# Kernel tuning notes

Hardware: AMD Instinct MI355X
Metric: run time of the kernel (lower is better)

Reference implementation:

```python
import jax, jax.numpy as jnp
import numpy as np

D_MODEL = 1024
NUM_HEADS = 16
D_HEAD = D_MODEL // NUM_HEADS
BATCH = 2
SEQ = 2048


def setup_inputs() -> dict:
    key = jax.random.key(0)
    ks = jax.random.split(key, 5)
    std = 0.02
    return {
        "x": jax.random.normal(ks[0], (BATCH, SEQ, D_MODEL), dtype=jnp.float32),
        "Wq": jax.random.normal(ks[1], (D_MODEL, D_MODEL), dtype=jnp.float32) * std,
        "Wk": jax.random.normal(ks[2], (D_MODEL, D_MODEL), dtype=jnp.float32) * std,
        "Wv": jax.random.normal(ks[3], (D_MODEL, D_MODEL), dtype=jnp.float32) * std,
        "Wo": jax.random.normal(ks[4], (D_MODEL, D_MODEL), dtype=jnp.float32) * std,
    }


def reference(x, Wq, Wk, Wv, Wo):
    batch, seq_len, d_model = x.shape
    h, dh = NUM_HEADS, D_HEAD

    def split_heads(W):
        # x @ W.T -> (b, s, d) -> (b, h, s, dh)
        p = jnp.einsum('bsd,ed->bse', x, W)
        return p.reshape(batch, seq_len, h, dh).transpose(0, 2, 1, 3)

    Q = split_heads(Wq)
    K = split_heads(Wk)
    V = split_heads(Wv)

    scale = 1.0 / jnp.sqrt(jnp.asarray(dh, dtype=x.dtype))
    scores = jnp.einsum('bhqd,bhkd->bhqk', Q, K) * scale
    causal = jnp.tril(jnp.ones((seq_len, seq_len), dtype=bool))
    scores = jnp.where(causal, scores, -jnp.inf)
    attn = jax.nn.softmax(scores, axis=-1)
    out = jnp.einsum('bhqk,bhkd->bhqd', attn, V)  # (b, h, s, dh)
    out = out.transpose(0, 2, 1, 3).reshape(batch, seq_len, d_model)
    return jnp.einsum('bsd,ed->bse', out, Wo)
```

## Files before the change

kernel.cpp:

```cpp
#include <hip/hip_runtime.h>

#define D_MODEL 1024
#define NUM_HEADS 16
#define D_HEAD 64
#define BATCH 2
#define SEQ 2048
#define MTOT (BATCH * SEQ)
#define PLANE ((size_t)MTOT * D_MODEL)
#define QSCALE 0.1803368801f

typedef unsigned short us;
typedef __bf16 bf16x8 __attribute__((ext_vector_type(8)));
typedef float floatx4 __attribute__((ext_vector_type(4)));

__device__ __forceinline__ unsigned int f2bf(float f) {
  union { float f; unsigned int i; } v; v.f = f;
  unsigned int r = v.i + 0x7FFFu + ((v.i >> 16) & 1u);
  return r >> 16;
}
__device__ __forceinline__ unsigned int f2bf_tr(float f) {
  union { float f; unsigned int i; } v; v.f = f;
  return v.i >> 16;
}

__global__ __launch_bounds__(256) void convert_all(const float* __restrict__ x,
                                                   const float* __restrict__ Wq,
                                                   const float* __restrict__ Wk,
                                                   const float* __restrict__ Wv,
                                                   us* __restrict__ xbf,
                                                   us* __restrict__ Wqkv) {
  const int i = blockIdx.x * 256 + threadIdx.x;
  const float* src;
  us* dst;
  if (i < (1 << 20)) {
    src = x + (size_t)i * 4;
    dst = xbf + (size_t)i * 4;
  } else {
    const int j = i - (1 << 20);
    const int w = j >> 18;
    const int o = j & ((1 << 18) - 1);
    const float* ws = (w == 0) ? Wq : (w == 1) ? Wk : Wv;
    src = ws + (size_t)o * 4;
    dst = Wqkv + (size_t)w * (D_MODEL * D_MODEL) + (size_t)o * 4;
  }
  float4 v = *(const float4*)src;
  uint2 pk;
  pk.x = f2bf(v.x) | (f2bf(v.y) << 16);
  pk.y = f2bf(v.z) | (f2bf(v.w) << 16);
  *(uint2*)dst = pk;
}

__global__ __launch_bounds__(256) void convert_bf16(const float* __restrict__ src,
                                                    us* __restrict__ dst, int n4) {
  int i = blockIdx.x * 256 + threadIdx.x;
  if (i >= n4) return;
  float4 v = *(const float4*)(src + (size_t)i * 4);
  uint2 pk;
  pk.x = f2bf(v.x) | (f2bf(v.y) << 16);
  pk.y = f2bf(v.z) | (f2bf(v.w) << 16);
  *(uint2*)(dst + (size_t)i * 4) = pk;
}

template <int CMODE>
__global__ __launch_bounds__(256) void gemm_mfma(const us* __restrict__ A,
                                                 const us* __restrict__ B,
                                                 void* __restrict__ Cv,
                                                 int M, int N, int K) {
  __shared__ __bf16 As[128 * 32];
  __shared__ __bf16 Bs[128 * 32];
  const int tid = threadIdx.x;
  const int wid = tid >> 6;
  const int lane = tid & 63;
  const int bm = blockIdx.y * 128;
  const int bn = blockIdx.x * 128;
  const int wm = (wid & 1) * 64;
  const int wn = (wid >> 1) * 64;
  const int lr = lane & 15;
  const int quad = lane >> 4;

  floatx4 acc[4][4] = {};
  const int cb0 = wid * 128;

  for (int k0 = 0; k0 < K; k0 += 32) {
    __syncthreads();
#pragma unroll
    for (int p = 0; p < 2; ++p) {
      const int cb = cb0 + p * 64;
      const int c = cb + lane;
      const us* ga = A + (size_t)(bm + (c >> 2)) * K + (k0 + (c & 3) * 8);
      const us* gb = B + (size_t)(bn + (c >> 2)) * K + (k0 + (c & 3) * 8);
      __builtin_amdgcn_global_load_lds((const __attribute__((address_space(1))) void*)ga,
                                       (__attribute__((address_space(3))) void*)(&As[cb * 8]),
                                       16, 0, 0);
      __builtin_amdgcn_global_load_lds((const __attribute__((address_space(1))) void*)gb,
                                       (__attribute__((address_space(3))) void*)(&Bs[cb * 8]),
                                       16, 0, 0);
    }
    __syncthreads();

    bf16x8 a[4], b[4];
#pragma unroll
    for (int i = 0; i < 4; ++i)
      a[i] = *(const bf16x8*)&As[(wm + i * 16 + lr) * 32 + quad * 8];
#pragma unroll
    for (int j = 0; j < 4; ++j)
      b[j] = *(const bf16x8*)&Bs[(wn + j * 16 + lr) * 32 + quad * 8];
#pragma unroll
    for (int i = 0; i < 4; ++i)
#pragma unroll
      for (int j = 0; j < 4; ++j)
        acc[i][j] = __builtin_amdgcn_mfma_f32_16x16x32_bf16(a[i], b[j], acc[i][j], 0, 0, 0);
  }

#pragma unroll
  for (int i = 0; i < 4; ++i) {
#pragma unroll
    for (int j = 0; j < 4; ++j) {
      const int col = bn + wn + j * 16 + lr;
      if constexpr (CMODE == 1) {
        us* dst = (us*)Cv;
        const int plane = col >> 10;
        if (plane < 2) {
          const float s = (plane == 0) ? QSCALE : 1.0f;
#pragma unroll
          for (int r = 0; r < 4; ++r) {
            const int row = bm + wm + i * 16 + quad * 4 + r;
            dst[(size_t)plane * PLANE + (size_t)row * 1024 + (col & 1023)] =
                (us)f2bf(acc[i][j][r] * s);
          }
        } else {
          const int d = col & 63;
          const int hh = (col >> 6) & 15;
          const int row0 = bm + wm + i * 16 + quad * 4;
          const int bb = row0 >> 11;
          const int ss = row0 & 2047;
          uint2 pk;
          pk.x = f2bf(acc[i][j][0]) | (f2bf(acc[i][j][1]) << 16);
          pk.y = f2bf(acc[i][j][2]) | (f2bf(acc[i][j][3]) << 16);
          *(uint2*)&dst[2 * PLANE + ((size_t)((bb * 16 + hh) * 64 + d)) * 2048 + ss] = pk;
        }
      } else {
#pragma unroll
        for (int r = 0; r < 4; ++r) {
          const int row = bm + wm + i * 16 + quad * 4 + r;
          ((float*)Cv)[(size_t)row * N + col] = acc[i][j][r];
        }
      }
    }
  }
}

#define ASTR 72

__global__ __launch_bounds__(256, 2) void attn_mfma(const us* __restrict__ Qb,
                                                    const us* __restrict__ Kb,
                                                    const us* __restrict__ Vtg,
                                                    us* __restrict__ Ob) {
  const int bx = blockIdx.x;
  const int b = bx >> 8;
  const int idx = bx & 255;
  const int h = idx >> 4;
  const int s0 = idx & 15;
  const int strip = b ? (15 - s0) : s0;
  const int q0 = strip * 128;
  const int ntiles = 2 * strip + 2;
  const int tid = threadIdx.x;
  const int w = tid >> 6;
  const int lane = tid & 63;
  const int lr = lane & 15;
  const int quad = lane >> 4;

  __shared__ us Ks[2][64 * ASTR];
  __shared__ us Vs[2][64 * ASTR];
  __shared__ us Ps[8 * 16 * ASTR];

  bf16x8 qa[2][2];
#pragma unroll
  for (int g = 0; g < 2; ++g) {
    const us* qp = Qb + (size_t)(b * SEQ + q0 + w * 32 + g * 16 + lr) * D_MODEL + h * D_HEAD;
    qa[g][0] = *(const bf16x8*)(qp + quad * 8);
    qa[g][1] = *(const bf16x8*)(qp + 32 + quad * 8);
  }

  floatx4 oacc[2][4] = {};
  floatx4 lacc[2] = {};
  bf16x8 ones;
#pragma unroll
  for (int i = 0; i < 8; ++i) ones[i] = (__bf16)1.0f;

  const us* kbase = Kb + (size_t)(b * SEQ) * D_MODEL + h * D_HEAD;
  const us* vbase = Vtg + (size_t)((b * 16 + h) * 64) * 2048;
  us* const pg0 = &Ps[(w * 2 + 0) * 16 * ASTR];
  us* const pg1 = &Ps[(w * 2 + 1) * 16 * ASTR];

  uint4 kreg[2], vreg[2];
#pragma unroll
  for (int p = 0; p < 2; ++p) {
    const int c = tid + 256 * p;
    kreg[p] = *(const uint4*)(kbase + (size_t)(c >> 3) * D_MODEL + (c & 7) * 8);
    vreg[p] = *(const uint4*)(vbase + (size_t)(c >> 3) * 2048 + (c & 7) * 8);
  }
#pragma unroll
  for (int p = 0; p < 2; ++p) {
    const int c = tid + 256 * p;
    *(uint4*)&Ks[0][(c >> 3) * ASTR + (c & 7) * 8] = kreg[p];
    *(uint4*)&Vs[0][(c >> 3) * ASTR + (c & 7) * 8] = vreg[p];
  }
  __syncthreads();

  for (int t = 0; t < ntiles; ++t) {
    const int k0 = t * 64;
    const int cur = t & 1;
    const bool more = (t + 1 < ntiles);

    if (more) {
      const int kn = k0 + 64;
#pragma unroll
      for (int p = 0; p < 2; ++p) {
        const int c = tid + 256 * p;
        kreg[p] = *(const uint4*)(kbase + (size_t)(kn + (c >> 3)) * D_MODEL + (c & 7) * 8);
        vreg[p] = *(const uint4*)(vbase + (size_t)(c >> 3) * 2048 + kn + (c & 7) * 8);
      }
    }

#pragma unroll
    for (int jt = 0; jt < 4; ++jt) {
      const bf16x8 kb0 = *(const bf16x8*)&Ks[cur][(jt * 16 + lr) * ASTR + quad * 8];
      const bf16x8 kb1 = *(const bf16x8*)&Ks[cur][(jt * 16 + lr) * ASTR + 32 + quad * 8];
#pragma unroll
      for (int g = 0; g < 2; ++g) {
        floatx4 s = {};
        s = __builtin_amdgcn_mfma_f32_16x16x32_bf16(kb0, qa[g][0], s, 0, 0, 0);
        s = __builtin_amdgcn_mfma_f32_16x16x32_bf16(kb1, qa[g][1], s, 0, 0, 0);
        const int grow = q0 + w * 32 + g * 16;
        const int kb = k0 + jt * 16 + quad * 4;
        const bool needMask = (k0 + jt * 16 + 15 > grow);
        float p[4];
#pragma unroll
        for (int r = 0; r < 4; ++r) {
          float e = __builtin_amdgcn_exp2f(s[r]);
          if (needMask && (kb + r > grow + lr)) e = 0.f;
          p[r] = e;
        }
        uint2 pk;
        pk.x = f2bf_tr(p[0]) | (f2bf_tr(p[1]) << 16);
        pk.y = f2bf_tr(p[2]) | (f2bf_tr(p[3]) << 16);
        us* const pg = g ? pg1 : pg0;
        *(uint2*)&pg[lr * ASTR + jt * 16 + quad * 4] = pk;
      }
    }

    const bf16x8 pa00 = *(const bf16x8*)&pg0[lr * ASTR + quad * 8];
    const bf16x8 pa01 = *(const bf16x8*)&pg0[lr * ASTR + 32 + quad * 8];
    const bf16x8 pa10 = *(const bf16x8*)&pg1[lr * ASTR + quad * 8];
    const bf16x8 pa11 = *(const bf16x8*)&pg1[lr * ASTR + 32 + quad * 8];
    lacc[0] = __builtin_amdgcn_mfma_f32_16x16x32_bf16(ones, pa00, lacc[0], 0, 0, 0);
    lacc[0] = __builtin_amdgcn_mfma_f32_16x16x32_bf16(ones, pa01, lacc[0], 0, 0, 0);
    lacc[1] = __builtin_amdgcn_mfma_f32_16x16x32_bf16(ones, pa10, lacc[1], 0, 0, 0);
    lacc[1] = __builtin_amdgcn_mfma_f32_16x16x32_bf16(ones, pa11, lacc[1], 0, 0, 0);
#pragma unroll
    for (int nt = 0; nt < 4; ++nt) {
      const bf16x8 vb0 = *(const bf16x8*)&Vs[cur][(nt * 16 + lr) * ASTR + quad * 8];
      const bf16x8 vb1 = *(const bf16x8*)&Vs[cur][(nt * 16 + lr) * ASTR + 32 + quad * 8];
      oacc[0][nt] = __builtin_amdgcn_mfma_f32_16x16x32_bf16(vb0, pa00, oacc[0][nt], 0, 0, 0);
      oacc[0][nt] = __builtin_amdgcn_mfma_f32_16x16x32_bf16(vb1, pa01, oacc[0][nt], 0, 0, 0);
      oacc[1][nt] = __builtin_amdgcn_mfma_f32_16x16x32_bf16(vb0, pa10, oacc[1][nt], 0, 0, 0);
      oacc[1][nt] = __builtin_amdgcn_mfma_f32_16x16x32_bf16(vb1, pa11, oacc[1][nt], 0, 0, 0);
    }

    if (more) {
      const int nxt = cur ^ 1;
#pragma unroll
      for (int p = 0; p < 2; ++p) {
        const int c = tid + 256 * p;
        *(uint4*)&Ks[nxt][(c >> 3) * ASTR + (c & 7) * 8] = kreg[p];
        *(uint4*)&Vs[nxt][(c >> 3) * ASTR + (c & 7) * 8] = vreg[p];
      }
    }
    __syncthreads();
  }

#pragma unroll
  for (int g = 0; g < 2; ++g) {
    us* const pg = g ? pg1 : pg0;
    const int grow = q0 + w * 32 + g * 16;
    const float inv = 1.f / lacc[g][0];
#pragma unroll
    for (int nt = 0; nt < 4; ++nt) {
      uint2 pk;
      pk.x = f2bf_tr(oacc[g][nt][0] * inv) | (f2bf_tr(oacc[g][nt][1] * inv) << 16);
      pk.y = f2bf_tr(oacc[g][nt][2] * inv) | (f2bf_tr(oacc[g][nt][3] * inv) << 16);
      *(uint2*)&pg[lr * ASTR + nt * 16 + quad * 4] = pk;
    }
#pragma unroll
    for (int p = 0; p < 2; ++p) {
      const int c = lane + 64 * p;
      *(uint4*)(Ob + (size_t)(b * SEQ + grow + (c >> 3)) * D_MODEL + h * D_HEAD + (c & 7) * 8) =
          *(const uint4*)&pg[(c >> 3) * ASTR + (c & 7) * 8];
    }
  }
}

extern "C" void kernel_launch(void* const* d_in, const int* in_sizes, int n_in,
                              void* d_out, int out_size, void* d_ws, size_t ws_size,
                              hipStream_t stream) {
  const float* x  = (const float*)d_in[0];
  const float* Wq = (const float*)d_in[1];
  const float* Wk = (const float*)d_in[2];
  const float* Wv = (const float*)d_in[3];
  const float* Wo = (const float*)d_in[4];

  us* xbf = (us*)d_ws;
  us* Qb  = xbf + PLANE;
  us* Kb  = xbf + 2 * PLANE;
  us* Vt  = xbf + 3 * PLANE;
  us* Ab  = xbf;
  us* Wqkv = (us*)d_out;
  us* Wobf = Qb;
  float* out = (float*)d_out;

  const int WN = D_MODEL * D_MODEL;

  convert_all<<<7168, 256, 0, stream>>>(x, Wq, Wk, Wv, xbf, Wqkv);

  gemm_mfma<1><<<dim3(3072 / 128, MTOT / 128), 256, 0, stream>>>(xbf, Wqkv, Qb, MTOT, 3072, D_MODEL);

  attn_mfma<<<512, 256, 0, stream>>>(Qb, Kb, Vt, Ab);

  convert_bf16<<<WN / 4 / 256, 256, 0, stream>>>(Wo, Wobf, WN / 4);
  gemm_mfma<2><<<dim3(D_MODEL / 128, MTOT / 128), 256, 0, stream>>>(Ab, Wobf, out, MTOT, D_MODEL, D_MODEL);
}
```

Baseline: 194.9 us.

## Process paired 64-row causal strips per block for balanced attention work

Each attention block used to handle one 128-row query strip, with strip order reversed across batches to spread load. Now each block handles two 64-row strips, s0 and 31-s0, one after the other, so every block does the same total number of KV tiles. Each wave now owns 16 query rows instead of 32, which halves the per-wave accumulators and the P scratch in shared memory. The cost is that each K/V tile loaded into shared memory now serves only 64 query rows instead of 128, so KV traffic per unit of compute roughly doubles.

Result: slower. 226.0 us (+16.0%).

```diff
diff --git a/kernel.cpp b/kernel.cpp
--- a/kernel.cpp
+++ b/kernel.cpp
@@ -157,13 +157,10 @@
                                                     const us* __restrict__ Vtg,
                                                     us* __restrict__ Ob) {
   const int bx = blockIdx.x;
-  const int b = bx >> 8;
-  const int idx = bx & 255;
-  const int h = idx >> 4;
-  const int s0 = idx & 15;
-  const int strip = b ? (15 - s0) : s0;
-  const int q0 = strip * 128;
-  const int ntiles = 2 * strip + 2;
+  const int s0 = bx & 15;
+  const int bh = bx >> 4;
+  const int b = bh >> 4;
+  const int h = bh & 15;
   const int tid = threadIdx.x;
   const int w = tid >> 6;
   const int lane = tid & 63;
@@ -172,67 +169,66 @@
 
   __shared__ us Ks[2][64 * ASTR];
   __shared__ us Vs[2][64 * ASTR];
-  __shared__ us Ps[8 * 16 * ASTR];
-
-  bf16x8 qa[2][2];
-#pragma unroll
-  for (int g = 0; g < 2; ++g) {
-    const us* qp = Qb + (size_t)(b * SEQ + q0 + w * 32 + g * 16 + lr) * D_MODEL + h * D_HEAD;
-    qa[g][0] = *(const bf16x8*)(qp + quad * 8);
-    qa[g][1] = *(const bf16x8*)(qp + 32 + quad * 8);
-  }
-
-  floatx4 oacc[2][4] = {};
-  floatx4 lacc[2] = {};
-  bf16x8 ones;
-#pragma unroll
-  for (int i = 0; i < 8; ++i) ones[i] = (__bf16)1.0f;
+  __shared__ us Ps[4 * 16 * ASTR];
 
   const us* kbase = Kb + (size_t)(b * SEQ) * D_MODEL + h * D_HEAD;
   const us* vbase = Vtg + (size_t)((b * 16 + h) * 64) * 2048;
-  us* const pg0 = &Ps[(w * 2 + 0) * 16 * ASTR];
-  us* const pg1 = &Ps[(w * 2 + 1) * 16 * ASTR];
-
-  uint4 kreg[2], vreg[2];
-#pragma unroll
-  for (int p = 0; p < 2; ++p) {
-    const int c = tid + 256 * p;
-    kreg[p] = *(const uint4*)(kbase + (size_t)(c >> 3) * D_MODEL + (c & 7) * 8);
-    vreg[p] = *(const uint4*)(vbase + (size_t)(c >> 3) * 2048 + (c & 7) * 8);
-  }
-#pragma unroll
-  for (int p = 0; p < 2; ++p) {
-    const int c = tid + 256 * p;
-    *(uint4*)&Ks[0][(c >> 3) * ASTR + (c & 7) * 8] = kreg[p];
-    *(uint4*)&Vs[0][(c >> 3) * ASTR + (c & 7) * 8] = vreg[p];
-  }
-  __syncthreads();
-
-  for (int t = 0; t < ntiles; ++t) {
-    const int k0 = t * 64;
-    const int cur = t & 1;
-    const bool more = (t + 1 < ntiles);
-
-    if (more) {
-      const int kn = k0 + 64;
-#pragma unroll
-      for (int p = 0; p < 2; ++p) {
-        const int c = tid + 256 * p;
-        kreg[p] = *(const uint4*)(kbase + (size_t)(kn + (c >> 3)) * D_MODEL + (c & 7) * 8);
-        vreg[p] = *(const uint4*)(vbase + (size_t)(c >> 3) * 2048 + kn + (c & 7) * 8);
-      }
-    }
-
-#pragma unroll
-    for (int jt = 0; jt < 4; ++jt) {
-      const bf16x8 kb0 = *(const bf16x8*)&Ks[cur][(jt * 16 + lr) * ASTR + quad * 8];
-      const bf16x8 kb1 = *(const bf16x8*)&Ks[cur][(jt * 16 + lr) * ASTR + 32 + quad * 8];
-#pragma unroll
-      for (int g = 0; g < 2; ++g) {
+  us* const pg = &Ps[w * 16 * ASTR];
+
+  bf16x8 ones;
+#pragma unroll
+  for (int i = 0; i < 8; ++i) ones[i] = (__bf16)1.0f;
+
+  for (int sp = 0; sp < 2; ++sp) {
+    const int strip = sp ? (31 - s0) : s0;
+    const int q0 = strip * 64;
+    const int ntiles = strip + 1;
+    const int grow = q0 + w * 16;
+
+    const us* qp = Qb + (size_t)(b * SEQ + grow + lr) * D_MODEL + h * D_HEAD;
+    const bf16x8 qa0 = *(const bf16x8*)(qp + quad * 8);
+    const bf16x8 qa1 = *(const bf16x8*)(qp + 32 + quad * 8);
+
+    floatx4 oacc[4] = {};
+    floatx4 lacc = {};
+
+    uint4 kreg[2], vreg[2];
+#pragma unroll
+    for (int p = 0; p < 2; ++p) {
+      const int c = tid + 256 * p;
+      kreg[p] = *(const uint4*)(kbase + (size_t)(c >> 3) * D_MODEL + (c & 7) * 8);
+      vreg[p] = *(const uint4*)(vbase + (size_t)(c >> 3) * 2048 + (c & 7) * 8);
+    }
+#pragma unroll
+    for (int p = 0; p < 2; ++p) {
+      const int c = tid + 256 * p;
+      *(uint4*)&Ks[0][(c >> 3) * ASTR + (c & 7) * 8] = kreg[p];
+      *(uint4*)&Vs[0][(c >> 3) * ASTR + (c & 7) * 8] = vreg[p];
+    }
+    __syncthreads();
+
+    for (int t = 0; t < ntiles; ++t) {
+      const int k0 = t * 64;
+      const int cur = t & 1;
+      const bool more = (t + 1 < ntiles);
+
+      if (more) {
+        const int kn = k0 + 64;
+#pragma unroll
+        for (int p = 0; p < 2; ++p) {
+          const int c = tid + 256 * p;
+          kreg[p] = *(const uint4*)(kbase + (size_t)(kn + (c >> 3)) * D_MODEL + (c & 7) * 8);
+          vreg[p] = *(const uint4*)(vbase + (size_t)(c >> 3) * 2048 + kn + (c & 7) * 8);
+        }
+      }
+
+#pragma unroll
+      for (int jt = 0; jt < 4; ++jt) {
+        const bf16x8 kb0 = *(const bf16x8*)&Ks[cur][(jt * 16 + lr) * ASTR + quad * 8];
+        const bf16x8 kb1 = *(const bf16x8*)&Ks[cur][(jt * 16 + lr) * ASTR + 32 + quad * 8];
         floatx4 s = {};
-        s = __builtin_amdgcn_mfma_f32_16x16x32_bf16(kb0, qa[g][0], s, 0, 0, 0);
-        s = __builtin_amdgcn_mfma_f32_16x16x32_bf16(kb1, qa[g][1], s, 0, 0, 0);
-        const int grow = q0 + w * 32 + g * 16;
+        s = __builtin_amdgcn_mfma_f32_16x16x32_bf16(kb0, qa0, s, 0, 0, 0);
+        s = __builtin_amdgcn_mfma_f32_16x16x32_bf16(kb1, qa1, s, 0, 0, 0);
         const int kb = k0 + jt * 16 + quad * 4;
         const bool needMask = (k0 + jt * 16 + 15 > grow);
         float p[4];
@@ -245,51 +241,39 @@
         uint2 pk;
         pk.x = f2bf_tr(p[0]) | (f2bf_tr(p[1]) << 16);
         pk.y = f2bf_tr(p[2]) | (f2bf_tr(p[3]) << 16);
-        us* const pg = g ? pg1 : pg0;
         *(uint2*)&pg[lr * ASTR + jt * 16 + quad * 4] = pk;
       }
-    }
-
-    const bf16x8 pa00 = *(const bf16x8*)&pg0[lr * ASTR + quad * 8];
-    const bf16x8 pa01 = *(const bf16x8*)&pg0[lr * ASTR + 32 + quad * 8];
-    const bf16x8 pa10 = *(const bf16x8*)&pg1[lr * ASTR + quad * 8];
-    const bf16x8 pa11 = *(const bf16x8*)&pg1[lr * ASTR + 32 + quad * 8];
-    lacc[0] = __builtin_amdgcn_mfma_f32_16x16x32_bf16(ones, pa00, lacc[0], 0, 0, 0);
-    lacc[0] = __builtin_amdgcn_mfma_f32_16x16x32_bf16(ones, pa01, lacc[0], 0, 0, 0);
-    lacc[1] = __builtin_amdgcn_mfma_f32_16x16x32_bf16(ones, pa10, lacc[1], 0, 0, 0);
-    lacc[1] = __builtin_amdgcn_mfma_f32_16x16x32_bf16(ones, pa11, lacc[1], 0, 0, 0);
-#pragma unroll
-    for (int nt = 0; nt < 4; ++nt) {
-      const bf16x8 vb0 = *(const bf16x8*)&Vs[cur][(nt * 16 + lr) * ASTR + quad * 8];
-      const bf16x8 vb1 = *(const bf16x8*)&Vs[cur][(nt * 16 + lr) * ASTR + 32 + quad * 8];
-      oacc[0][nt] = __builtin_amdgcn_mfma_f32_16x16x32_bf16(vb0, pa00, oacc[0][nt], 0, 0, 0);
-      oacc[0][nt] = __builtin_amdgcn_mfma_f32_16x16x32_bf16(vb1, pa01, oacc[0][nt], 0, 0, 0);
-      oacc[1][nt] = __builtin_amdgcn_mfma_f32_16x16x32_bf16(vb0, pa10, oacc[1][nt], 0, 0, 0);
-      oacc[1][nt] = __builtin_amdgcn_mfma_f32_16x16x32_bf16(vb1, pa11, oacc[1][nt], 0, 0, 0);
-    }
-
-    if (more) {
-      const int nxt = cur ^ 1;
-#pragma unroll
-      for (int p = 0; p < 2; ++p) {
-        const int c = tid + 256 * p;
-        *(uint4*)&Ks[nxt][(c >> 3) * ASTR + (c & 7) * 8] = kreg[p];
-        *(uint4*)&Vs[nxt][(c >> 3) * ASTR + (c & 7) * 8] = vreg[p];
-      }
-    }
-    __syncthreads();
-  }
-
-#pragma unroll
-  for (int g = 0; g < 2; ++g) {
-    us* const pg = g ? pg1 : pg0;
-    const int grow = q0 + w * 32 + g * 16;
-    const float inv = 1.f / lacc[g][0];
+
+      const bf16x8 pa0 = *(const bf16x8*)&pg[lr * ASTR + quad * 8];
+      const bf16x8 pa1 = *(const bf16x8*)&pg[lr * ASTR + 32 + quad * 8];
+      lacc = __builtin_amdgcn_mfma_f32_16x16x32_bf16(ones, pa0, lacc, 0, 0, 0);
+      lacc = __builtin_amdgcn_mfma_f32_16x16x32_bf16(ones, pa1, lacc, 0, 0, 0);
+#pragma unroll
+      for (int nt = 0; nt < 4; ++nt) {
+        const bf16x8 vb0 = *(const bf16x8*)&Vs[cur][(nt * 16 + lr) * ASTR + quad * 8];
+        const bf16x8 vb1 = *(const bf16x8*)&Vs[cur][(nt * 16 + lr) * ASTR + 32 + quad * 8];
+        oacc[nt] = __builtin_amdgcn_mfma_f32_16x16x32_bf16(vb0, pa0, oacc[nt], 0, 0, 0);
+        oacc[nt] = __builtin_amdgcn_mfma_f32_16x16x32_bf16(vb1, pa1, oacc[nt], 0, 0, 0);
+      }
+
+      if (more) {
+        const int nxt = cur ^ 1;
+#pragma unroll
+        for (int p = 0; p < 2; ++p) {
+          const int c = tid + 256 * p;
+          *(uint4*)&Ks[nxt][(c >> 3) * ASTR + (c & 7) * 8] = kreg[p];
+          *(uint4*)&Vs[nxt][(c >> 3) * ASTR + (c & 7) * 8] = vreg[p];
+        }
+      }
+      __syncthreads();
+    }
+
+    const float inv = 1.f / lacc[0];
 #pragma unroll
     for (int nt = 0; nt < 4; ++nt) {
       uint2 pk;
-      pk.x = f2bf_tr(oacc[g][nt][0] * inv) | (f2bf_tr(oacc[g][nt][1] * inv) << 16);
-      pk.y = f2bf_tr(oacc[g][nt][2] * inv) | (f2bf_tr(oacc[g][nt][3] * inv) << 16);
+      pk.x = f2bf_tr(oacc[nt][0] * inv) | (f2bf_tr(oacc[nt][1] * inv) << 16);
+      pk.y = f2bf_tr(oacc[nt][2] * inv) | (f2bf_tr(oacc[nt][3] * inv) << 16);
       *(uint2*)&pg[lr * ASTR + nt * 16 + quad * 4] = pk;
     }
 #pragma unroll
```

## Make attention kernel persistent with atomic longest-first job queue

Applied to the files above, without the earlier changes.

The attention kernel becomes persistent. 256 blocks each pull (strip, batch, head) jobs from a global atomic counter, ordered so the longest causal strips go first, and the counter is reset inside the conversion kernel. The aim is to balance uneven causal workloads across CUs and remove tail imbalance from static block scheduling. In exchange, the grid is halved, which may cut resident waves per CU and latency hiding. It also adds an atomic plus a barrier per job, and keeps the counter in scratch space inside the output buffer.

New measurement: 226.4 us. 1.16x slower.

```diff
diff --git a/kernel.cpp b/kernel.cpp
--- a/kernel.cpp
+++ b/kernel.cpp
@@ -28,8 +28,10 @@
                                                    const float* __restrict__ Wk,
                                                    const float* __restrict__ Wv,
                                                    us* __restrict__ xbf,
-                                                   us* __restrict__ Wqkv) {
+                                                   us* __restrict__ Wqkv,
+                                                   int* __restrict__ ctr) {
   const int i = blockIdx.x * 256 + threadIdx.x;
+  if (i == 0) *ctr = 0;
   const float* src;
   us* dst;
   if (i < (1 << 20)) {
@@ -151,19 +153,13 @@
 }
 
 #define ASTR 72
+#define NJOBS 512
 
 __global__ __launch_bounds__(256, 2) void attn_mfma(const us* __restrict__ Qb,
                                                     const us* __restrict__ Kb,
                                                     const us* __restrict__ Vtg,
-                                                    us* __restrict__ Ob) {
-  const int bx = blockIdx.x;
-  const int b = bx >> 8;
-  const int idx = bx & 255;
-  const int h = idx >> 4;
-  const int s0 = idx & 15;
-  const int strip = b ? (15 - s0) : s0;
-  const int q0 = strip * 128;
-  const int ntiles = 2 * strip + 2;
+                                                    us* __restrict__ Ob,
+                                                    int* __restrict__ ctr) {
   const int tid = threadIdx.x;
   const int w = tid >> 6;
   const int lane = tid & 63;
@@ -173,130 +169,146 @@
   __shared__ us Ks[2][64 * ASTR];
   __shared__ us Vs[2][64 * ASTR];
   __shared__ us Ps[8 * 16 * ASTR];
-
-  bf16x8 qa[2][2];
-#pragma unroll
-  for (int g = 0; g < 2; ++g) {
-    const us* qp = Qb + (size_t)(b * SEQ + q0 + w * 32 + g * 16 + lr) * D_MODEL + h * D_HEAD;
-    qa[g][0] = *(const bf16x8*)(qp + quad * 8);
-    qa[g][1] = *(const bf16x8*)(qp + 32 + quad * 8);
-  }
-
-  floatx4 oacc[2][4] = {};
-  floatx4 lacc[2] = {};
-  bf16x8 ones;
-#pragma unroll
-  for (int i = 0; i < 8; ++i) ones[i] = (__bf16)1.0f;
-
-  const us* kbase = Kb + (size_t)(b * SEQ) * D_MODEL + h * D_HEAD;
-  const us* vbase = Vtg + (size_t)((b * 16 + h) * 64) * 2048;
+  __shared__ int jslot;
+
   us* const pg0 = &Ps[(w * 2 + 0) * 16 * ASTR];
   us* const pg1 = &Ps[(w * 2 + 1) * 16 * ASTR];
 
-  uint4 kreg[2], vreg[2];
-#pragma unroll
-  for (int p = 0; p < 2; ++p) {
-    const int c = tid + 256 * p;
-    kreg[p] = *(const uint4*)(kbase + (size_t)(c >> 3) * D_MODEL + (c & 7) * 8);
-    vreg[p] = *(const uint4*)(vbase + (size_t)(c >> 3) * 2048 + (c & 7) * 8);
-  }
-#pragma unroll
-  for (int p = 0; p < 2; ++p) {
-    const int c = tid + 256 * p;
-    *(uint4*)&Ks[0][(c >> 3) * ASTR + (c & 7) * 8] = kreg[p];
-    *(uint4*)&Vs[0][(c >> 3) * ASTR + (c & 7) * 8] = vreg[p];
-  }
-  __syncthreads();
-
-  for (int t = 0; t < ntiles; ++t) {
-    const int k0 = t * 64;
-    const int cur = t & 1;
-    const bool more = (t + 1 < ntiles);
-
-    if (more) {
-      const int kn = k0 + 64;
+  bf16x8 ones;
+#pragma unroll
+  for (int i = 0; i < 8; ++i) ones[i] = (__bf16)1.0f;
+
+  for (;;) {
+    if (tid == 0) jslot = atomicAdd(ctr, 1);
+    __syncthreads();
+    const int job = jslot;
+    if (job >= NJOBS) break;
+    const int strip = 15 - (job >> 5);
+    const int slot = job & 31;
+    const int b = slot >> 4;
+    const int h = slot & 15;
+    const int q0 = strip * 128;
+    const int ntiles = 2 * strip + 2;
+
+    const us* kbase = Kb + (size_t)(b * SEQ) * D_MODEL + h * D_HEAD;
+    const us* vbase = Vtg + (size_t)((b * 16 + h) * 64) * 2048;
+
+    bf16x8 qa[2][2];
+#pragma unroll
+    for (int g = 0; g < 2; ++g) {
+      const us* qp = Qb + (size_t)(b * SEQ + q0 + w * 32 + g * 16 + lr) * D_MODEL + h * D_HEAD;
+      qa[g][0] = *(const bf16x8*)(qp + quad * 8);
+      qa[g][1] = *(const bf16x8*)(qp + 32 + quad * 8);
+    }
+
+    floatx4 oacc[2][4] = {};
+    floatx4 lacc[2] = {};
+
+    uint4 kreg[2], vreg[2];
+#pragma unroll
+    for (int p = 0; p < 2; ++p) {
+      const int c = tid + 256 * p;
+      kreg[p] = *(const uint4*)(kbase + (size_t)(c >> 3) * D_MODEL + (c & 7) * 8);
+      vreg[p] = *(const uint4*)(vbase + (size_t)(c >> 3) * 2048 + (c & 7) * 8);
+    }
+#pragma unroll
+    for (int p = 0; p < 2; ++p) {
+      const int c = tid + 256 * p;
+      *(uint4*)&Ks[0][(c >> 3) * ASTR + (c & 7) * 8] = kreg[p];
+      *(uint4*)&Vs[0][(c >> 3) * ASTR + (c & 7) * 8] = vreg[p];
+    }
+    __syncthreads();
+
+    for (int t = 0; t < ntiles; ++t) {
+      const int k0 = t * 64;
+      const int cur = t & 1;
+      const bool more = (t + 1 < ntiles);
+
+      if (more) {
+        const int kn = k0 + 64;
+#pragma unroll
+        for (int p = 0; p < 2; ++p) {
+          const int c = tid + 256 * p;
+          kreg[p] = *(const uint4*)(kbase + (size_t)(kn + (c >> 3)) * D_MODEL + (c & 7) * 8);
+          vreg[p] = *(const uint4*)(vbase + (size_t)(c >> 3) * 2048 + kn + (c & 7) * 8);
+        }
+      }
+
+#pragma unroll
+      for (int jt = 0; jt < 4; ++jt) {
+        const bf16x8 kb0 = *(const bf16x8*)&Ks[cur][(jt * 16 + lr) * ASTR + quad * 8];
+        const bf16x8 kb1 = *(const bf16x8*)&Ks[cur][(jt * 16 + lr) * ASTR + 32 + quad * 8];
+#pragma unroll
+        for (int g = 0; g < 2; ++g) {
+          floatx4 s = {};
+          s = __builtin_amdgcn_mfma_f32_16x16x32_bf16(kb0, qa[g][0], s, 0, 0, 0);
+          s = __builtin_amdgcn_mfma_f32_16x16x32_bf16(kb1, qa[g][1], s, 0, 0, 0);
+          const int grow = q0 + w * 32 + g * 16;
+          const int kb = k0 + jt * 16 + quad * 4;
+          const bool needMask = (k0 + jt * 16 + 15 > grow);
+          float p[4];
+#pragma unroll
+          for (int r = 0; r < 4; ++r) {
+            float e = __builtin_amdgcn_exp2f(s[r]);
+            if (needMask && (kb + r > grow + lr)) e = 0.f;
+            p[r] = e;
+          }
+          uint2 pk;
+          pk.x = f2bf_tr(p[0]) | (f2bf_tr(p[1]) << 16);
+          pk.y = f2bf_tr(p[2]) | (f2bf_tr(p[3]) << 16);
+          us* const pg = g ? pg1 : pg0;
+          *(uint2*)&pg[lr * ASTR + jt * 16 + quad * 4] = pk;
+        }
+      }
+
+      const bf16x8 pa00 = *(const bf16x8*)&pg0[lr * ASTR + quad * 8];
+      const bf16x8 pa01 = *(const bf16x8*)&pg0[lr * ASTR + 32 + quad * 8];
+      const bf16x8 pa10 = *(const bf16x8*)&pg1[lr * ASTR + quad * 8];
+      const bf16x8 pa11 = *(const bf16x8*)&pg1[lr * ASTR + 32 + quad * 8];
+      lacc[0] = __builtin_amdgcn_mfma_f32_16x16x32_bf16(ones, pa00, lacc[0], 0, 0, 0);
+      lacc[0] = __builtin_amdgcn_mfma_f32_16x16x32_bf16(ones, pa01, lacc[0], 0, 0, 0);
+      lacc[1] = __builtin_amdgcn_mfma_f32_16x16x32_bf16(ones, pa10, lacc[1], 0, 0, 0);
+      lacc[1] = __builtin_amdgcn_mfma_f32_16x16x32_bf16(ones, pa11, lacc[1], 0, 0, 0);
+#pragma unroll
+      for (int nt = 0; nt < 4; ++nt) {
+        const bf16x8 vb0 = *(const bf16x8*)&Vs[cur][(nt * 16 + lr) * ASTR + quad * 8];
+        const bf16x8 vb1 = *(const bf16x8*)&Vs[cur][(nt * 16 + lr) * ASTR + 32 + quad * 8];
+        oacc[0][nt] = __builtin_amdgcn_mfma_f32_16x16x32_bf16(vb0, pa00, oacc[0][nt], 0, 0, 0);
+        oacc[0][nt] = __builtin_amdgcn_mfma_f32_16x16x32_bf16(vb1, pa01, oacc[0][nt], 0, 0, 0);
+        oacc[1][nt] = __builtin_amdgcn_mfma_f32_16x16x32_bf16(vb0, pa10, oacc[1][nt], 0, 0, 0);
+        oacc[1][nt] = __builtin_amdgcn_mfma_f32_16x16x32_bf16(vb1, pa11, oacc[1][nt], 0, 0, 0);
+      }
+
+      if (more) {
+        const int nxt = cur ^ 1;
+#pragma unroll
+        for (int p = 0; p < 2; ++p) {
+          const int c = tid + 256 * p;
+          *(uint4*)&Ks[nxt][(c >> 3) * ASTR + (c & 7) * 8] = kreg[p];
+          *(uint4*)&Vs[nxt][(c >> 3) * ASTR + (c & 7) * 8] = vreg[p];
+        }
+      }
+      __syncthreads();
+    }
+
+#pragma unroll
+    for (int g = 0; g < 2; ++g) {
+      us* const pg = g ? pg1 : pg0;
+      const int grow = q0 + w * 32 + g * 16;
+      const float inv = 1.f / lacc[g][0];
+#pragma unroll
+      for (int nt = 0; nt < 4; ++nt) {
+        uint2 pk;
+        pk.x = f2bf_tr(oacc[g][nt][0] * inv) | (f2bf_tr(oacc[g][nt][1] * inv) << 16);
+        pk.y = f2bf_tr(oacc[g][nt][2] * inv) | (f2bf_tr(oacc[g][nt][3] * inv) << 16);
+        *(uint2*)&pg[lr * ASTR + nt * 16 + quad * 4] = pk;
+      }
 #pragma unroll
       for (int p = 0; p < 2; ++p) {
-        const int c = tid + 256 * p;
-        kreg[p] = *(const uint4*)(kbase + (size_t)(kn + (c >> 3)) * D_MODEL + (c & 7) * 8);
-        vreg[p] = *(const uint4*)(vbase + (size_t)(c >> 3) * 2048 + kn + (c & 7) * 8);
-      }
-    }
-
-#pragma unroll
-    for (int jt = 0; jt < 4; ++jt) {
-      const bf16x8 kb0 = *(const bf16x8*)&Ks[cur][(jt * 16 + lr) * ASTR + quad * 8];
-      const bf16x8 kb1 = *(const bf16x8*)&Ks[cur][(jt * 16 + lr) * ASTR + 32 + quad * 8];
-#pragma unroll
-      for (int g = 0; g < 2; ++g) {
-        floatx4 s = {};
-        s = __builtin_amdgcn_mfma_f32_16x16x32_bf16(kb0, qa[g][0], s, 0, 0, 0);
-        s = __builtin_amdgcn_mfma_f32_16x16x32_bf16(kb1, qa[g][1], s, 0, 0, 0);
-        const int grow = q0 + w * 32 + g * 16;
-        const int kb = k0 + jt * 16 + quad * 4;
-        const bool needMask = (k0 + jt * 16 + 15 > grow);
-        float p[4];
-#pragma unroll
-        for (int r = 0; r < 4; ++r) {
-          float e = __builtin_amdgcn_exp2f(s[r]);
-          if (needMask && (kb + r > grow + lr)) e = 0.f;
-          p[r] = e;
-        }
-        uint2 pk;
-        pk.x = f2bf_tr(p[0]) | (f2bf_tr(p[1]) << 16);
-        pk.y = f2bf_tr(p[2]) | (f2bf_tr(p[3]) << 16);
-        us* const pg = g ? pg1 : pg0;
-        *(uint2*)&pg[lr * ASTR + jt * 16 + quad * 4] = pk;
-      }
-    }
-
-    const bf16x8 pa00 = *(const bf16x8*)&pg0[lr * ASTR + quad * 8];
-    const bf16x8 pa01 = *(const bf16x8*)&pg0[lr * ASTR + 32 + quad * 8];
-    const bf16x8 pa10 = *(const bf16x8*)&pg1[lr * ASTR + quad * 8];
-    const bf16x8 pa11 = *(const bf16x8*)&pg1[lr * ASTR + 32 + quad * 8];
-    lacc[0] = __builtin_amdgcn_mfma_f32_16x16x32_bf16(ones, pa00, lacc[0], 0, 0, 0);
-    lacc[0] = __builtin_amdgcn_mfma_f32_16x16x32_bf16(ones, pa01, lacc[0], 0, 0, 0);
-    lacc[1] = __builtin_amdgcn_mfma_f32_16x16x32_bf16(ones, pa10, lacc[1], 0, 0, 0);
-    lacc[1] = __builtin_amdgcn_mfma_f32_16x16x32_bf16(ones, pa11, lacc[1], 0, 0, 0);
-#pragma unroll
-    for (int nt = 0; nt < 4; ++nt) {
-      const bf16x8 vb0 = *(const bf16x8*)&Vs[cur][(nt * 16 + lr) * ASTR + quad * 8];
-      const bf16x8 vb1 = *(const bf16x8*)&Vs[cur][(nt * 16 + lr) * ASTR + 32 + quad * 8];
-      oacc[0][nt] = __builtin_amdgcn_mfma_f32_16x16x32_bf16(vb0, pa00, oacc[0][nt], 0, 0, 0);
-      oacc[0][nt] = __builtin_amdgcn_mfma_f32_16x16x32_bf16(vb1, pa01, oacc[0][nt], 0, 0, 0);
-      oacc[1][nt] = __builtin_amdgcn_mfma_f32_16x16x32_bf16(vb0, pa10, oacc[1][nt], 0, 0, 0);
-      oacc[1][nt] = __builtin_amdgcn_mfma_f32_16x16x32_bf16(vb1, pa11, oacc[1][nt], 0, 0, 0);
-    }
-
-    if (more) {
-      const int nxt = cur ^ 1;
-#pragma unroll
-      for (int p = 0; p < 2; ++p) {
-        const int c = tid + 256 * p;
-        *(uint4*)&Ks[nxt][(c >> 3) * ASTR + (c & 7) * 8] = kreg[p];
-        *(uint4*)&Vs[nxt][(c >> 3) * ASTR + (c & 7) * 8] = vreg[p];
-      }
-    }
-    __syncthreads();
-  }
-
-#pragma unroll
-  for (int g = 0; g < 2; ++g) {
-    us* const pg = g ? pg1 : pg0;
-    const int grow = q0 + w * 32 + g * 16;
-    const float inv = 1.f / lacc[g][0];
-#pragma unroll
-    for (int nt = 0; nt < 4; ++nt) {
-      uint2 pk;
-      pk.x = f2bf_tr(oacc[g][nt][0] * inv) | (f2bf_tr(oacc[g][nt][1] * inv) << 16);
-      pk.y = f2bf_tr(oacc[g][nt][2] * inv) | (f2bf_tr(oacc[g][nt][3] * inv) << 16);
-      *(uint2*)&pg[lr * ASTR + nt * 16 + quad * 4] = pk;
-    }
-#pragma unroll
-    for (int p = 0; p < 2; ++p) {
-      const int c = lane + 64 * p;
-      *(uint4*)(Ob + (size_t)(b * SEQ + grow + (c >> 3)) * D_MODEL + h * D_HEAD + (c & 7) * 8) =
-          *(const uint4*)&pg[(c >> 3) * ASTR + (c & 7) * 8];
+        const int c = lane + 64 * p;
+        *(uint4*)(Ob + (size_t)(b * SEQ + grow + (c >> 3)) * D_MODEL + h * D_HEAD + (c & 7) * 8) =
+            *(const uint4*)&pg[(c >> 3) * ASTR + (c & 7) * 8];
+      }
     }
   }
 }
@@ -316,16 +328,17 @@
   us* Vt  = xbf + 3 * PLANE;
   us* Ab  = xbf;
   us* Wqkv = (us*)d_out;
+  int* ctr = (int*)((char*)d_out + (8u << 20));
   us* Wobf = Qb;
   float* out = (float*)d_out;
 
   const int WN = D_MODEL * D_MODEL;
 
-  convert_all<<<7168, 256, 0, stream>>>(x, Wq, Wk, Wv, xbf, Wqkv);
+  convert_all<<<7168, 256, 0, stream>>>(x, Wq, Wk, Wv, xbf, Wqkv, ctr);
 
   gemm_mfma<1><<<dim3(3072 / 128, MTOT / 128), 256, 0, stream>>>(xbf, Wqkv, Qb, MTOT, 3072, D_MODEL);
 
-  attn_mfma<<<512, 256, 0, stream>>>(Qb, Kb, Vt, Ab);
+  attn_mfma<<<256, 256, 0, stream>>>(Qb, Kb, Vt, Ab, ctr);
 
   convert_bf16<<<WN / 4 / 256, 256, 0, stream>>>(Wo, Wobf, WN / 4);
   gemm_mfma<2><<<dim3(D_MODEL / 128, MTOT / 128), 256, 0, stream>>>(Ab, Wobf, out, MTOT, D_MODEL, D_MODEL);
```
